# Optimization experiments

Measured on AMD Instinct MI355X. Metric: run time of the kernel, lower is better.

## Reference

```python
import jax, jax.numpy as jnp
import numpy as np

N, M, D = 6144, 6144, 128
EPS = 1e-12


def setup_inputs() -> dict:
    key = jax.random.key(0)
    k1, k2 = jax.random.split(key)
    desc1 = jax.random.normal(k1, (N, D), dtype=jnp.float32)
    desc2 = jax.random.normal(k2, (M, D), dtype=jnp.float32)
    # DISK descriptors are unit-normalized; distances in the docstring are in [0, 2]
    desc1 = desc1 / jnp.linalg.norm(desc1, axis=-1, keepdims=True)
    desc2 = desc2 / jnp.linalg.norm(desc2, axis=-1, keepdims=True)
    inverse_T = jnp.asarray(15.0, dtype=jnp.float32)  # learned scalar nn.Parameter
    return {"desc1": desc1, "desc2": desc2, "inverse_T": inverse_T}


def reference(desc1, desc2, inverse_T):
    # pairwise Euclidean distance matrix [N, M]
    sq1 = jnp.sum(desc1 * desc1, axis=-1)            # [N]
    sq2 = jnp.sum(desc2 * desc2, axis=-1)            # [M]
    inner = desc1 @ desc2.T                           # [N, M] GEMM, D=128
    d2 = sq1[:, None] + sq2[None, :] - 2.0 * inner
    distances = jnp.sqrt(jnp.maximum(d2, 0.0) + EPS)  # [N, M]

    affinity = -inverse_T * distances                 # scaled logits

    # Categorical(logits=affinity).logits  == log_softmax over rows
    # Categorical(logits=affinity.T).logits.T == log_softmax over columns
    logp_I = jax.nn.log_softmax(affinity, axis=1)     # row distribution [N, M]
    logp_T = jax.nn.log_softmax(affinity, axis=0)     # col distribution [N, M]

    dense_logp = logp_I + logp_T                      # dual-softmax log prob
    dense_p = jnp.exp(logp_I) * jnp.exp(logp_T)       # dual-softmax prob

    # mle(): argmax matches with cycle-consistency check
    maxes_I = jnp.argmax(affinity, axis=1)            # [N] best col per row
    maxes_T = jnp.argmax(affinity, axis=0)            # [M] best row per col
    idx = jnp.arange(N)
    cycle_consistent = maxes_T[maxes_I] == idx        # [N] bool mask
    # Original returns stack([right[paired_left], paired_left]) over the
    # consistent subset; here we keep fixed shape [2, N] + the mask
    # (matches[:, i] valid iff cycle_consistent[i]).
    matches = jnp.stack([idx, maxes_I], axis=0)       # [2, N] int

    return dense_logp, dense_p, matches, cycle_consistent
```

## Files before the change

### kernel.cpp

```cpp
#include <hip/hip_runtime.h>
#include <hip/hip_bf16.h>
#include <stdint.h>

#define NROWS 6144
#define MCOLS 6144
#define DDIM  128
#define EPSQ  1e-12f
#define NTC   48

typedef unsigned long long ull;
typedef __attribute__((ext_vector_type(8))) short short8;
typedef __attribute__((ext_vector_type(4))) float floatx4;

__device__ __forceinline__ ull makeKey(float v, int idx) {
    unsigned u = __float_as_uint(v);
    u = (u & 0x80000000u) ? ~u : (u | 0x80000000u);
    return ((ull)u << 32) | (ull)(0xFFFFFFFFu - (unsigned)idx);
}
__device__ __forceinline__ int decodeKeyIdx(ull k) {
    return (int)(0xFFFFFFFFu - (unsigned)(k & 0xFFFFFFFFull));
}
__device__ __forceinline__ unsigned short f2bf(float f) {
    unsigned u = __float_as_uint(f);
    u += 0x7fffu + ((u >> 16) & 1);
    return (unsigned short)(u >> 16);
}

#define DPPF(x, ctrl) __uint_as_float(__builtin_amdgcn_update_dpp( \
    0, (int)__float_as_uint(x), (ctrl), 0xF, 0xF, false))
#define DPPI(x, ctrl) __builtin_amdgcn_update_dpp(0, (x), (ctrl), 0xF, 0xF, false)
#define ROR8 0x128
#define ROR4 0x124
#define ROR2 0x122
#define ROR1 0x121

#define GLOAD16(g, l) \
  __builtin_amdgcn_global_load_lds((const __attribute__((address_space(1))) unsigned int*)(g), \
                                   (__attribute__((address_space(3))) unsigned int*)(l), 16, 0, 0)

__device__ __forceinline__ void tileCoord(int& rowBase, int& colBase) {
    int id  = blockIdx.x;
    int wid = (id & 7) * (NTC * NTC / 8) + (id >> 3);
    rowBase = (wid / NTC) * 128;
    colBase = (wid % NTC) * 128;
}

__global__ __launch_bounds__(256) void convert_kernel(
    const float* __restrict__ d1, const float* __restrict__ d2,
    unsigned short* __restrict__ s1, unsigned short* __restrict__ s2,
    float* __restrict__ sq1, float* __restrict__ sq2,
    unsigned* __restrict__ zero_region)
{
    int tid = blockIdx.x * 256 + threadIdx.x;
    if (tid < 36864) zero_region[tid] = 0u;

    int gw = tid >> 6;
    int lane = threadIdx.x & 63;
    if (gw >= NROWS + MCOLS) return;
    bool isA = gw < NROWS;
    int row = isA ? gw : gw - NROWS;
    const float* src = (isA ? d1 : d2) + (size_t)row * DDIM;
    unsigned short* dst = (isA ? s1 : s2) + (size_t)row * 256;

    float2 v = *(const float2*)(src + lane * 2);
    float s = v.x * v.x + v.y * v.y;
    #pragma unroll
    for (int m = 1; m < 64; m <<= 1) s += __shfl_xor(s, m, 64);
    if (lane == 0) { if (isA) sq1[row] = s; else sq2[row] = s; }

    unsigned short h0 = f2bf(v.x), h1 = f2bf(v.y);
    float r0 = v.x - __uint_as_float((unsigned)h0 << 16);
    float r1 = v.y - __uint_as_float((unsigned)h1 << 16);
    unsigned short l0 = f2bf(r0), l1 = f2bf(r1);
    int c  = lane >> 5;
    int e  = (2 * lane) & 63;
    int pe = e ^ ((row & 7) << 3);
    *(unsigned*)(dst + c * 128 + pe)      = (unsigned)h0 | ((unsigned)h1 << 16);
    *(unsigned*)(dst + c * 128 + 64 + pe) = (unsigned)l0 | ((unsigned)l1 << 16);
}

__device__ __forceinline__ void stageBuf(
    const unsigned short* __restrict__ gpanel, unsigned short* buf,
    int c, int h, int t)
{
    #pragma unroll
    for (int it = 0; it < 2; ++it) {
        int li = t * 8 + it * 4096;
        int r  = li >> 6, e = li & 63;
        int gi = r * 256 + c * 128 + h * 64 + e;
        GLOAD16(gpanel + gi, &buf[li]);
    }
}

__device__ __forceinline__ void computeSplit(
    const unsigned short* Ab_, const unsigned short* Bb_,
    int lane, int wr, int wc, floatx4 acc[4][2])
{
    const int l15 = lane & 15;
    const int q16 = (lane >> 4) * 16;
    const int sw  = (l15 & 7) << 4;
    const char* Ab = (const char*)Ab_;
    const char* Bb = (const char*)Bb_;
    #pragma unroll
    for (int ks = 0; ks < 2; ++ks) {
        const int kk = (ks * 64 + q16) ^ sw;
        short8 af[4], bf[2];
        #pragma unroll
        for (int mi = 0; mi < 4; ++mi)
            af[mi] = *(const short8*)(Ab + (wr * 64 + mi * 16 + l15) * 128 + kk);
        #pragma unroll
        for (int ni = 0; ni < 2; ++ni)
            bf[ni] = *(const short8*)(Bb + (wc * 32 + ni * 16 + l15) * 128 + kk);
        #pragma unroll
        for (int mi = 0; mi < 4; ++mi)
            #pragma unroll
            for (int ni = 0; ni < 2; ++ni)
                acc[mi][ni] = __builtin_amdgcn_mfma_f32_16x16x32_bf16(
                    bf[ni], af[mi], acc[mi][ni], 0, 0, 0);
    }
}

__global__ __launch_bounds__(512, 4) void gemm_reduce_kernel(
    const unsigned short* __restrict__ s1, const unsigned short* __restrict__ s2,
    const float* __restrict__ invT,
    const float* __restrict__ sq1, const float* __restrict__ sq2,
    float* __restrict__ rowsum, float* __restrict__ colsum,
    ull* __restrict__ rowkey, ull* __restrict__ colkey)
{
    __shared__ unsigned short A0[8192], A1[8192], B0[8192], B1[8192];
    __shared__ float lRowS[128], lColS[128];
    __shared__ ull   lRowK[128], lColK[128];

    const int t = threadIdx.x;
    const int lane = t & 63;
    const int wave = t >> 6;
    const int wr = wave >> 2, wc = wave & 3;
    int rowBase, colBase;
    tileCoord(rowBase, colBase);
    const unsigned short* gA = s1 + (size_t)rowBase * 256;
    const unsigned short* gB = s2 + (size_t)colBase * 256;

    if (t < 128) { lRowS[t] = 0.f; lColS[t] = 0.f; lRowK[t] = 0ull; lColK[t] = 0ull; }

    floatx4 acc[4][2] = {};
    stageBuf(gA, A0, 0, 0, t); stageBuf(gB, B0, 0, 0, t);
    __syncthreads();
    stageBuf(gA, A1, 0, 1, t); stageBuf(gB, B1, 0, 1, t);
    computeSplit(A0, B0, lane, wr, wc, acc);
    __syncthreads();
    computeSplit(A0, B1, lane, wr, wc, acc);
    __syncthreads();
    stageBuf(gA, A0, 1, 0, t); stageBuf(gB, B1, 1, 0, t);
    computeSplit(A1, B0, lane, wr, wc, acc);
    __syncthreads();
    stageBuf(gA, A1, 1, 1, t); stageBuf(gB, B0, 1, 1, t);
    computeSplit(A0, B1, lane, wr, wc, acc);
    __syncthreads();
    computeSplit(A0, B0, lane, wr, wc, acc);
    computeSplit(A1, B1, lane, wr, wc, acc);

    const int l15 = lane & 15;
    const int q   = lane >> 4;
    const float iT = *invT;
    float s1r[4];
    #pragma unroll
    for (int mi = 0; mi < 4; ++mi)
        s1r[mi] = sq1[rowBase + wr * 64 + mi * 16 + l15] + EPSQ;
    const int colLoc0 = wc * 32 + q * 4;
    float4 s2v[2];
    #pragma unroll
    for (int ni = 0; ni < 2; ++ni)
        s2v[ni] = *(const float4*)(sq2 + colBase + colLoc0 + ni * 16);

    float rs[4], rv[4]; int rj[4];
    float cs[2][4], cv[2][4]; int ci[2][4];
    #pragma unroll
    for (int ni = 0; ni < 2; ++ni)
        #pragma unroll
        for (int r = 0; r < 4; ++r) { cs[ni][r] = 0.f; cv[ni][r] = -1e30f; ci[ni][r] = 0; }

    #pragma unroll
    for (int mi = 0; mi < 4; ++mi) {
        const int gi = rowBase + wr * 64 + mi * 16 + l15;
        rs[mi] = 0.f; rv[mi] = -1e30f; rj[mi] = 0;
        #pragma unroll
        for (int ni = 0; ni < 2; ++ni) {
            #pragma unroll
            for (int r = 0; r < 4; ++r) {
                float sv2 = (r == 0) ? s2v[ni].x : (r == 1) ? s2v[ni].y
                          : (r == 2) ? s2v[ni].z : s2v[ni].w;
                float dd = s1r[mi] + sv2 - 2.0f * acc[mi][ni][r];
                float v = -iT * __builtin_amdgcn_sqrtf(fmaxf(dd, EPSQ));
                float e = __expf(v);
                rs[mi] += e;
                if (v > rv[mi]) { rv[mi] = v; rj[mi] = colBase + colLoc0 + ni * 16 + r; }
                cs[ni][r] += e;
                if (v > cv[ni][r]) { cv[ni][r] = v; ci[ni][r] = gi; }
            }
        }
    }

    #pragma unroll
    for (int mi = 0; mi < 4; ++mi) {
        float s = rs[mi];
        s += __shfl_xor(s, 16, 64); s += __shfl_xor(s, 32, 64);
        float v = rv[mi];
        v = fmaxf(v, __shfl_xor(v, 16, 64)); v = fmaxf(v, __shfl_xor(v, 32, 64));
        int cand = (rv[mi] == v) ? rj[mi] : 0x7FFFFFFF;
        cand = min(cand, __shfl_xor(cand, 16, 64));
        cand = min(cand, __shfl_xor(cand, 32, 64));
        if (lane < 16) {
            int idx = wr * 64 + mi * 16 + l15;
            atomicAdd(&lRowS[idx], s);
            atomicMax(&lRowK[idx], makeKey(v, cand));
        }
    }

    #pragma unroll
    for (int ni = 0; ni < 2; ++ni)
        #pragma unroll
        for (int r = 0; r < 4; ++r) {
            float s = cs[ni][r];
            s += DPPF(s, ROR8); s += DPPF(s, ROR4); s += DPPF(s, ROR2); s += DPPF(s, ROR1);
            float v = cv[ni][r];
            v = fmaxf(v, DPPF(v, ROR8)); v = fmaxf(v, DPPF(v, ROR4));
            v = fmaxf(v, DPPF(v, ROR2)); v = fmaxf(v, DPPF(v, ROR1));
            int cand = (cv[ni][r] == v) ? ci[ni][r] : 0x7FFFFFFF;
            cand = min(cand, DPPI(cand, ROR8)); cand = min(cand, DPPI(cand, ROR4));
            cand = min(cand, DPPI(cand, ROR2)); cand = min(cand, DPPI(cand, ROR1));
            if (l15 == 0) {
                int idx = colLoc0 + ni * 16 + r;
                atomicAdd(&lColS[idx], s);
                atomicMax(&lColK[idx], makeKey(v, cand));
            }
        }
    __syncthreads();

    if (t < 128) {
        atomicAdd(&rowsum[rowBase + t], lRowS[t]);
        atomicMax(&rowkey[rowBase + t], lRowK[t]);
    } else if (t < 256) {
        int j = t - 128;
        atomicAdd(&colsum[colBase + j], lColS[j]);
        atomicMax(&colkey[colBase + j], lColK[j]);
    }
}

__global__ __launch_bounds__(256) void finalize_small_kernel(
    const float* __restrict__ rowsum, const ull* __restrict__ rowkey,
    const float* __restrict__ colsum, const ull* __restrict__ colkey,
    float* __restrict__ rowlse, float* __restrict__ collse,
    float* __restrict__ out_matches, float* __restrict__ out_cyc)
{
    int i = blockIdx.x * 256 + threadIdx.x;
    if (i >= NROWS) return;
    rowlse[i] = logf(rowsum[i]);
    collse[i] = logf(colsum[i]);
    int mi = decodeKeyIdx(rowkey[i]);
    out_matches[i]         = (float)i;
    out_matches[NROWS + i] = (float)mi;
    out_cyc[i] = (decodeKeyIdx(colkey[mi]) == i) ? 1.0f : 0.0f;
}

#define VSTRIDE 132
__global__ __launch_bounds__(512, 4) void gemm_write_kernel(
    const unsigned short* __restrict__ s1, const unsigned short* __restrict__ s2,
    const float* __restrict__ invT,
    const float* __restrict__ sq1, const float* __restrict__ sq2,
    const float* __restrict__ rowlse, const float* __restrict__ collse,
    float* __restrict__ logp_out, float* __restrict__ p_out)
{
    __shared__ char SMEM[128 * VSTRIDE * 4];
    unsigned short* A0 = (unsigned short*)(SMEM);
    unsigned short* A1 = (unsigned short*)(SMEM + 16384);
    unsigned short* B0 = (unsigned short*)(SMEM + 32768);
    unsigned short* B1 = (unsigned short*)(SMEM + 49152);
    float* V = (float*)SMEM;

    const int t = threadIdx.x;
    const int lane = t & 63;
    const int wave = t >> 6;
    const int wr = wave >> 2, wc = wave & 3;
    int rowBase, colBase;
    tileCoord(rowBase, colBase);
    const unsigned short* gA = s1 + (size_t)rowBase * 256;
    const unsigned short* gB = s2 + (size_t)colBase * 256;

    floatx4 acc[4][2] = {};
    stageBuf(gA, A0, 0, 0, t); stageBuf(gB, B0, 0, 0, t);
    __syncthreads();
    stageBuf(gA, A1, 0, 1, t); stageBuf(gB, B1, 1, 0, t);
    computeSplit(A0, B0, lane, wr, wc, acc);
    __syncthreads();
    stageBuf(gA, A0, 1, 0, t);
    computeSplit(A1, B0, lane, wr, wc, acc);
    __syncthreads();
    stageBuf(gA, A1, 1, 1, t);
    computeSplit(A0, B1, lane, wr, wc, acc);
    __syncthreads();
    computeSplit(A1, B1, lane, wr, wc, acc);

    const int l15 = lane & 15;
    const int q   = lane >> 4;
    const float iT = *invT;
    float s1r[4];
    #pragma unroll
    for (int mi = 0; mi < 4; ++mi)
        s1r[mi] = sq1[rowBase + wr * 64 + mi * 16 + l15] + EPSQ;
    const int colLoc0 = wc * 32 + q * 4;
    float4 s2v[2];
    #pragma unroll
    for (int ni = 0; ni < 2; ++ni)
        s2v[ni] = *(const float4*)(sq2 + colBase + colLoc0 + ni * 16);

    __syncthreads();
    #pragma unroll
    for (int mi = 0; mi < 4; ++mi) {
        const int lrow = wr * 64 + mi * 16 + l15;
        #pragma unroll
        for (int ni = 0; ni < 2; ++ni) {
            floatx4 vv;
            #pragma unroll
            for (int r = 0; r < 4; ++r) {
                float sv2 = (r == 0) ? s2v[ni].x : (r == 1) ? s2v[ni].y
                          : (r == 2) ? s2v[ni].z : s2v[ni].w;
                float dd = s1r[mi] + sv2 - 2.0f * acc[mi][ni][r];
                vv[r] = -iT * __builtin_amdgcn_sqrtf(fmaxf(dd, EPSQ));
            }
            *(floatx4*)(V + lrow * VSTRIDE + colLoc0 + ni * 16) = vv;
        }
    }
    __syncthreads();

    const int rsub = lane >> 4;
    const int csub = (lane & 15) * 4;
    #pragma unroll
    for (int g = 0; g < 4; ++g) {
        const int lrow = wave * 16 + g * 4 + rsub;
        const int grow = rowBase + lrow;
        const float rl = rowlse[grow];
        #pragma unroll
        for (int h = 0; h < 2; ++h) {
            const int lcol = h * 64 + csub;
            float4 cl = *(const float4*)(collse + colBase + lcol);
            float4 v4 = *(const float4*)(V + lrow * VSTRIDE + lcol);
            floatx4 ov, pv;
            ov[0] = (v4.x - rl) + (v4.x - cl.x); pv[0] = __expf(ov[0]);
            ov[1] = (v4.y - rl) + (v4.y - cl.y); pv[1] = __expf(ov[1]);
            ov[2] = (v4.z - rl) + (v4.z - cl.z); pv[2] = __expf(ov[2]);
            ov[3] = (v4.w - rl) + (v4.w - cl.w); pv[3] = __expf(ov[3]);
            size_t off = (size_t)grow * MCOLS + colBase + lcol;
            __builtin_nontemporal_store(ov, (floatx4*)(logp_out + off));
            __builtin_nontemporal_store(pv, (floatx4*)(p_out + off));
        }
    }
}

extern "C" void kernel_launch(void* const* d_in, const int* in_sizes, int n_in,
                              void* d_out, int out_size, void* d_ws, size_t ws_size,
                              hipStream_t stream) {
    const float* d1   = (const float*)d_in[0];
    const float* d2   = (const float*)d_in[1];
    const float* invT = (const float*)d_in[2];

    float* out     = (float*)d_out;
    float* logp    = out;
    float* pout    = out + (size_t)NROWS * MCOLS;
    float* matches = out + 2ull * NROWS * MCOLS;
    float* cyc     = matches + 2 * NROWS;

    char* ws = (char*)d_ws;
    float* rowsum = (float*)(ws + 0);
    float* colsum = (float*)(ws + 24576);
    ull*   rowkey = (ull*)(ws + 49152);
    ull*   colkey = (ull*)(ws + 98304);
    float* sq1    = (float*)(ws + 147456);
    float* sq2    = (float*)(ws + 172032);
    float* rowlse = (float*)(ws + 196608);
    float* collse = (float*)(ws + 221184);
    unsigned short* s1 = (unsigned short*)(ws + 270336);
    unsigned short* s2 = (unsigned short*)(ws + 270336 + 3145728);

    convert_kernel<<<(NROWS + MCOLS) / 4, 256, 0, stream>>>(
        d1, d2, s1, s2, sq1, sq2, (unsigned*)ws);

    gemm_reduce_kernel<<<NTC * NTC, 512, 0, stream>>>(
        s1, s2, invT, sq1, sq2, rowsum, colsum, rowkey, colkey);

    finalize_small_kernel<<<NROWS / 256, 256, 0, stream>>>(
        rowsum, rowkey, colsum, colkey, rowlse, collse, matches, cyc);

    gemm_write_kernel<<<NTC * NTC, 512, 0, stream>>>(
        s1, s2, invT, sq1, sq2, rowlse, collse, logp, pout);
}
```

Measured before the change: 130.8 us.

## Fuse finalize into write kernel, vectorize convert, merge first GEMM stage

Removes the separate finalize kernel by computing log-sums inline in the write kernel and emitting matches and cycle flags from the column-0 tiles. The convert kernel is restructured to 16 threads per row with 8-wide vector loads and stores. The reduce GEMM prologue stages both B halves up front and merges two compute steps, dropping one barrier. In exchange, logf is recomputed redundantly per tile instead of once per row and column.

```diff
diff --git a/kernel.cpp b/kernel.cpp
--- a/kernel.cpp
+++ b/kernel.cpp
@@ -54,29 +54,37 @@
     int tid = blockIdx.x * 256 + threadIdx.x;
     if (tid < 36864) zero_region[tid] = 0u;
 
-    int gw = tid >> 6;
-    int lane = threadIdx.x & 63;
-    if (gw >= NROWS + MCOLS) return;
-    bool isA = gw < NROWS;
-    int row = isA ? gw : gw - NROWS;
-    const float* src = (isA ? d1 : d2) + (size_t)row * DDIM;
-    unsigned short* dst = (isA ? s1 : s2) + (size_t)row * 256;
-
-    float2 v = *(const float2*)(src + lane * 2);
-    float s = v.x * v.x + v.y * v.y;
-    #pragma unroll
-    for (int m = 1; m < 64; m <<= 1) s += __shfl_xor(s, m, 64);
-    if (lane == 0) { if (isA) sq1[row] = s; else sq2[row] = s; }
-
-    unsigned short h0 = f2bf(v.x), h1 = f2bf(v.y);
-    float r0 = v.x - __uint_as_float((unsigned)h0 << 16);
-    float r1 = v.y - __uint_as_float((unsigned)h1 << 16);
-    unsigned short l0 = f2bf(r0), l1 = f2bf(r1);
-    int c  = lane >> 5;
-    int e  = (2 * lane) & 63;
-    int pe = e ^ ((row & 7) << 3);
-    *(unsigned*)(dst + c * 128 + pe)      = (unsigned)h0 | ((unsigned)h1 << 16);
-    *(unsigned*)(dst + c * 128 + 64 + pe) = (unsigned)l0 | ((unsigned)l1 << 16);
+    int row = tid >> 4;
+    int sub = tid & 15;
+    if (row >= NROWS + MCOLS) return;
+    bool isA = row < NROWS;
+    int r = isA ? row : row - NROWS;
+    const float* src = (isA ? d1 : d2) + (size_t)r * DDIM + sub * 8;
+    unsigned short* dst = (isA ? s1 : s2) + (size_t)r * 256;
+
+    float4 v0 = *(const float4*)(src);
+    float4 v1 = *(const float4*)(src + 4);
+    float vs[8] = {v0.x, v0.y, v0.z, v0.w, v1.x, v1.y, v1.z, v1.w};
+
+    float s = 0.f;
+    #pragma unroll
+    for (int j = 0; j < 8; ++j) s += vs[j] * vs[j];
+    #pragma unroll
+    for (int m = 1; m < 16; m <<= 1) s += __shfl_xor(s, m, 64);
+    if (sub == 0) { if (isA) sq1[r] = s; else sq2[r] = s; }
+
+    short8 hi, lo;
+    #pragma unroll
+    for (int j = 0; j < 8; ++j) {
+        unsigned short h = f2bf(vs[j]);
+        hi[j] = (short)h;
+        lo[j] = (short)f2bf(vs[j] - __uint_as_float((unsigned)h << 16));
+    }
+    int e  = sub * 8;
+    int c  = e >> 6;
+    int pe = (e & 63) ^ ((r & 7) << 3);
+    *(short8*)(dst + c * 128 + pe)      = hi;
+    *(short8*)(dst + c * 128 + 64 + pe) = lo;
 }
 
 __device__ __forceinline__ void stageBuf(
@@ -117,6 +125,43 @@
             for (int ni = 0; ni < 2; ++ni)
                 acc[mi][ni] = __builtin_amdgcn_mfma_f32_16x16x32_bf16(
                     bf[ni], af[mi], acc[mi][ni], 0, 0, 0);
+    }
+}
+
+__device__ __forceinline__ void computeSplitAB2(
+    const unsigned short* Ab_, const unsigned short* B0_, const unsigned short* B1_,
+    int lane, int wr, int wc, floatx4 acc[4][2])
+{
+    const int l15 = lane & 15;
+    const int q16 = (lane >> 4) * 16;
+    const int sw  = (l15 & 7) << 4;
+    const char* Ab = (const char*)Ab_;
+    const char* B0 = (const char*)B0_;
+    const char* B1 = (const char*)B1_;
+    #pragma unroll
+    for (int ks = 0; ks < 2; ++ks) {
+        const int kk = (ks * 64 + q16) ^ sw;
+        short8 af[4], bf0[2], bf1[2];
+        #pragma unroll
+        for (int mi = 0; mi < 4; ++mi)
+            af[mi] = *(const short8*)(Ab + (wr * 64 + mi * 16 + l15) * 128 + kk);
+        #pragma unroll
+        for (int ni = 0; ni < 2; ++ni) {
+            bf0[ni] = *(const short8*)(B0 + (wc * 32 + ni * 16 + l15) * 128 + kk);
+            bf1[ni] = *(const short8*)(B1 + (wc * 32 + ni * 16 + l15) * 128 + kk);
+        }
+        #pragma unroll
+        for (int mi = 0; mi < 4; ++mi)
+            #pragma unroll
+            for (int ni = 0; ni < 2; ++ni)
+                acc[mi][ni] = __builtin_amdgcn_mfma_f32_16x16x32_bf16(
+                    bf0[ni], af[mi], acc[mi][ni], 0, 0, 0);
+        #pragma unroll
+        for (int mi = 0; mi < 4; ++mi)
+            #pragma unroll
+            for (int ni = 0; ni < 2; ++ni)
+                acc[mi][ni] = __builtin_amdgcn_mfma_f32_16x16x32_bf16(
+                    bf1[ni], af[mi], acc[mi][ni], 0, 0, 0);
     }
 }
 
@@ -143,12 +188,10 @@
     if (t < 128) { lRowS[t] = 0.f; lColS[t] = 0.f; lRowK[t] = 0ull; lColK[t] = 0ull; }
 
     floatx4 acc[4][2] = {};
-    stageBuf(gA, A0, 0, 0, t); stageBuf(gB, B0, 0, 0, t);
-    __syncthreads();
-    stageBuf(gA, A1, 0, 1, t); stageBuf(gB, B1, 0, 1, t);
-    computeSplit(A0, B0, lane, wr, wc, acc);
-    __syncthreads();
-    computeSplit(A0, B1, lane, wr, wc, acc);
+    stageBuf(gA, A0, 0, 0, t); stageBuf(gB, B0, 0, 0, t); stageBuf(gB, B1, 0, 1, t);
+    __syncthreads();
+    stageBuf(gA, A1, 0, 1, t);
+    computeSplitAB2(A0, B0, B1, lane, wr, wc, acc);
     __syncthreads();
     stageBuf(gA, A0, 1, 0, t); stageBuf(gB, B1, 1, 0, t);
     computeSplit(A1, B0, lane, wr, wc, acc);
@@ -246,29 +289,15 @@
     }
 }
 
-__global__ __launch_bounds__(256) void finalize_small_kernel(
-    const float* __restrict__ rowsum, const ull* __restrict__ rowkey,
-    const float* __restrict__ colsum, const ull* __restrict__ colkey,
-    float* __restrict__ rowlse, float* __restrict__ collse,
-    float* __restrict__ out_matches, float* __restrict__ out_cyc)
-{
-    int i = blockIdx.x * 256 + threadIdx.x;
-    if (i >= NROWS) return;
-    rowlse[i] = logf(rowsum[i]);
-    collse[i] = logf(colsum[i]);
-    int mi = decodeKeyIdx(rowkey[i]);
-    out_matches[i]         = (float)i;
-    out_matches[NROWS + i] = (float)mi;
-    out_cyc[i] = (decodeKeyIdx(colkey[mi]) == i) ? 1.0f : 0.0f;
-}
-
 #define VSTRIDE 132
 __global__ __launch_bounds__(512, 4) void gemm_write_kernel(
     const unsigned short* __restrict__ s1, const unsigned short* __restrict__ s2,
     const float* __restrict__ invT,
     const float* __restrict__ sq1, const float* __restrict__ sq2,
-    const float* __restrict__ rowlse, const float* __restrict__ collse,
-    float* __restrict__ logp_out, float* __restrict__ p_out)
+    const float* __restrict__ rowsum, const float* __restrict__ colsum,
+    const ull* __restrict__ rowkey, const ull* __restrict__ colkey,
+    float* __restrict__ logp_out, float* __restrict__ p_out,
+    float* __restrict__ out_matches, float* __restrict__ out_cyc)
 {
     __shared__ char SMEM[128 * VSTRIDE * 4];
     unsigned short* A0 = (unsigned short*)(SMEM);
@@ -285,6 +314,14 @@
     tileCoord(rowBase, colBase);
     const unsigned short* gA = s1 + (size_t)rowBase * 256;
     const unsigned short* gB = s2 + (size_t)colBase * 256;
+
+    if (colBase == 0 && t < 128) {
+        int i = rowBase + t;
+        int mi = decodeKeyIdx(rowkey[i]);
+        out_matches[i]         = (float)i;
+        out_matches[NROWS + i] = (float)mi;
+        out_cyc[i] = (decodeKeyIdx(colkey[mi]) == i) ? 1.0f : 0.0f;
+    }
 
     floatx4 acc[4][2] = {};
     stageBuf(gA, A0, 0, 0, t); stageBuf(gB, B0, 0, 0, t);
@@ -338,11 +375,14 @@
     for (int g = 0; g < 4; ++g) {
         const int lrow = wave * 16 + g * 4 + rsub;
         const int grow = rowBase + lrow;
-        const float rl = rowlse[grow];
+        const float rl = logf(rowsum[grow]);
         #pragma unroll
         for (int h = 0; h < 2; ++h) {
             const int lcol = h * 64 + csub;
-            float4 cl = *(const float4*)(collse + colBase + lcol);
+            float4 csum = *(const float4*)(colsum + colBase + lcol);
+            float4 cl;
+            cl.x = logf(csum.x); cl.y = logf(csum.y);
+            cl.z = logf(csum.z); cl.w = logf(csum.w);
             float4 v4 = *(const float4*)(V + lrow * VSTRIDE + lcol);
             floatx4 ov, pv;
             ov[0] = (v4.x - rl) + (v4.x - cl.x); pv[0] = __expf(ov[0]);
@@ -376,20 +416,16 @@
     ull*   colkey = (ull*)(ws + 98304);
     float* sq1    = (float*)(ws + 147456);
     float* sq2    = (float*)(ws + 172032);
-    float* rowlse = (float*)(ws + 196608);
-    float* collse = (float*)(ws + 221184);
     unsigned short* s1 = (unsigned short*)(ws + 270336);
     unsigned short* s2 = (unsigned short*)(ws + 270336 + 3145728);
 
-    convert_kernel<<<(NROWS + MCOLS) / 4, 256, 0, stream>>>(
+    convert_kernel<<<(NROWS + MCOLS) * 16 / 256, 256, 0, stream>>>(
         d1, d2, s1, s2, sq1, sq2, (unsigned*)ws);
 
     gemm_reduce_kernel<<<NTC * NTC, 512, 0, stream>>>(
         s1, s2, invT, sq1, sq2, rowsum, colsum, rowkey, colkey);
 
-    finalize_small_kernel<<<NROWS / 256, 256, 0, stream>>>(
-        rowsum, rowkey, colsum, colkey, rowlse, collse, matches, cyc);
-
     gemm_write_kernel<<<NTC * NTC, 512, 0, stream>>>(
-        s1, s2, invT, sq1, sq2, rowlse, collse, logp, pout);
-}
+        s1, s2, invT, sq1, sq2, rowsum, colsum, rowkey, colkey,
+        logp, pout, matches, cyc);
+}
```

Measured after the change: 127.9 us (median of 2 runs). 2.2% less time.
